# Performance work log

Hardware: AMD Instinct MI355X
Metric: run time of the kernel (lower is better)

Reference implementation:

```python
import jax, jax.numpy as jnp
import numpy as np

EPS = 1e-12  # guard sqrt at zero distance


def setup_inputs() -> dict:
    key = jax.random.key(0)
    k1, k2 = jax.random.split(key)
    B, C, N = 4, 3, 8192
    predict_pc = jax.random.normal(k1, (B, C, N), dtype=jnp.float32)
    gt_pc = jax.random.normal(k2, (B, C, N), dtype=jnp.float32)
    return {"predict_pc": predict_pc, "gt_pc": gt_pc}


def reference(predict_pc, gt_pc):
    # predict_pc: [B, 3, Np], gt_pc: [B, 3, Ng]
    B = gt_pc.shape[0]
    Np = predict_pc.shape[2]
    Ng = gt_pc.shape[2]
    denom = B * (Ng + Np)

    # Pairwise Euclidean distances d[b, n, m] = ||predict[b,:,n] - gt[b,:,m]||
    # via the |p|^2 + |g|^2 - 2 p.g expansion (avoids [B,3,Np,Ng] intermediate).
    p2 = jnp.sum(predict_pc * predict_pc, axis=1)            # [B, Np]
    g2 = jnp.sum(gt_pc * gt_pc, axis=1)                      # [B, Ng]
    dot = jnp.einsum('bcn,bcm->bnm', predict_pc, gt_pc)      # [B, Np, Ng]
    d2 = p2[:, :, None] + g2[:, None, :] - 2.0 * dot         # [B, Np, Ng]
    d = jnp.sqrt(jnp.maximum(d2, EPS))

    # z: for each gt point, distance to nearest predicted point -> min over Np
    z = jnp.min(d, axis=1)   # [B, Ng]
    # z_2: for each predicted point, distance to nearest gt point -> min over Ng
    z2 = jnp.min(d, axis=2)  # [B, Np]

    loss = z.sum() / denom + z2.sum() / denom
    return loss
```

## Files before the change

kernel.cpp:

```cpp
#include <hip/hip_runtime.h>
#include <math.h>


#define B_       4
#define N_       8192
#define THREADS  256
#define RX       8
#define XB       (THREADS * RX)
#define XBLKS    (N_ / XB)
#define NPB      (2 * B_)
#define RTHREADS 128

typedef float v2f __attribute__((ext_vector_type(2)));

__device__ __forceinline__ v2f pk_fma(v2f a, v2f b, v2f c) {
    v2f d;
    asm("v_pk_fma_f32 %0, %1, %2, %3" : "=v"(d) : "v"(a), "v"(b), "v"(c));
    return d;
}

__device__ __forceinline__ float min3f(float a, float b, float c) {
    float d;
    asm("v_min3_f32 %0, %1, %2, %3" : "=v"(d) : "v"(a), "v"(b), "v"(c));
    return d;
}


template<int YSPL>
__global__ __launch_bounds__(THREADS)
void chamfer_sweep_t(const float* __restrict__ P, const float* __restrict__ G,
                     float* __restrict__ partial)
{
    constexpr int YCHUNK = N_ / YSPL;
    constexpr int NJJ    = YCHUNK / 2;
    __shared__ float4 ytile[2 * NJJ];

    const int t      = threadIdx.x;
    const int xblk   = blockIdx.x;
    const int ysplit = blockIdx.y;
    const int bz     = blockIdx.z;
    const int pass   = bz >> 2;
    const int b      = bz & 3;

    const float* Xb = (pass ? G : P) + (size_t)b * 3 * N_;
    const float* Yb = (pass ? P : G) + (size_t)b * 3 * N_;

    const int ybase = ysplit * YCHUNK;
    if (t < NJJ) {
        const int n0 = ybase + 2 * t;
        float2 x01 = *(const float2*)&Yb[n0];
        float2 y01 = *(const float2*)&Yb[N_ + n0];
        float2 z01 = *(const float2*)&Yb[2 * N_ + n0];
        float w0 = fmaf(x01.x, x01.x, fmaf(y01.x, y01.x, z01.x * z01.x));
        float w1 = fmaf(x01.y, x01.y, fmaf(y01.y, y01.y, z01.y * z01.y));
        ytile[2 * t]     = make_float4(x01.x, x01.y, y01.x, y01.y);
        ytile[2 * t + 1] = make_float4(z01.x, z01.y, w0, w1);
    }

    const int xbase = xblk * XB;
    v2f m2x2[RX], m2y2[RX], m2z2[RX];
    float mn[RX];
#pragma unroll
    for (int r = 0; r < RX; ++r) {
        const int n = xbase + r * THREADS + t;
        float px = Xb[n];
        float py = Xb[N_ + n];
        float pz = Xb[2 * N_ + n];
        float ax = -2.0f * px, ay = -2.0f * py, az = -2.0f * pz;
        m2x2[r] = (v2f){ax, ax};
        m2y2[r] = (v2f){ay, ay};
        m2z2[r] = (v2f){az, az};
        mn[r]   = 3.4e38f;
    }
    __syncthreads();

#pragma unroll
    for (int jj = 0; jj < NJJ; ++jj) {
        float4 a4 = ytile[2 * jj];
        float4 b4 = ytile[2 * jj + 1];
        v2f gx2 = (v2f){a4.x, a4.y};
        v2f gy2 = (v2f){a4.z, a4.w};
        v2f gz2 = (v2f){b4.x, b4.y};
        v2f gw2 = (v2f){b4.z, b4.w};
#pragma unroll
        for (int r = 0; r < RX; ++r) {
            v2f s = pk_fma(m2z2[r], gz2, gw2);
            s = pk_fma(m2y2[r], gy2, s);
            s = pk_fma(m2x2[r], gx2, s);
            mn[r] = min3f(mn[r], s.x, s.y);
        }
    }

    float* pout = partial + ((size_t)bz * YSPL + ysplit) * N_ + xbase;
#pragma unroll
    for (int r = 0; r < RX; ++r) {
        float ax = m2x2[r].x, ay = m2y2[r].x, az = m2z2[r].x;
        float p2 = 0.25f * fmaf(ax, ax, fmaf(ay, ay, az * az));
        pout[r * THREADS + t] = fmaxf(mn[r] + p2, 1e-12f);
    }
}

template<int YSPL>
__global__ __launch_bounds__(RTHREADS)
void chamfer_reduce1_t(const float* __restrict__ partial,
                       float* __restrict__ gsum2)
{
    __shared__ float red[RTHREADS];
    const int g  = blockIdx.x * RTHREADS + threadIdx.x;
    const int pb = g >> 11;
    const int xq = g & 2047;
    const float4* p = (const float4*)(partial + (size_t)pb * YSPL * N_) + xq;
    float4 m = p[0];
#pragma unroll
    for (int ys = 1; ys < YSPL; ++ys) {
        float4 v = p[(size_t)ys * (N_ / 4)];
        m.x = fminf(m.x, v.x); m.y = fminf(m.y, v.y);
        m.z = fminf(m.z, v.z); m.w = fminf(m.w, v.w);
    }
    red[threadIdx.x] = sqrtf(m.x) + sqrtf(m.y) + sqrtf(m.z) + sqrtf(m.w);
    __syncthreads();
    for (int off = RTHREADS / 2; off > 0; off >>= 1) {
        if (threadIdx.x < off) red[threadIdx.x] += red[threadIdx.x + off];
        __syncthreads();
    }
    if (threadIdx.x == 0) gsum2[blockIdx.x] = red[0];
}

__global__ __launch_bounds__(RTHREADS)
void chamfer_final_kernel(const float* __restrict__ gsum2, float* __restrict__ out)
{
    __shared__ float red[RTHREADS];
    red[threadIdx.x] = gsum2[threadIdx.x];
    __syncthreads();
    for (int off = RTHREADS / 2; off > 0; off >>= 1) {
        if (threadIdx.x < off) red[threadIdx.x] += red[threadIdx.x + off];
        __syncthreads();
    }
    if (threadIdx.x == 0) out[0] = red[0] * (1.0f / 65536.0f);
}

#define LRX      8
#define LXB      (THREADS * LRX)
#define LXBLKS   (N_ / LXB)
#define LYSPL    32
#define LYCHUNK  (N_ / LYSPL)
#define LNGROUPS (2 * B_ * LXBLKS)
#define POISON   0xAAAAAAAAu

__global__ __launch_bounds__(THREADS)
void chamfer_fused_kernel(const float* __restrict__ P, const float* __restrict__ G,
                          unsigned* __restrict__ mins, unsigned* __restrict__ gcnt,
                          unsigned* __restrict__ fcnt, float* __restrict__ gsum,
                          float* __restrict__ out)
{
    __shared__ float4 ytile[2 * (LYCHUNK / 2)];
    __shared__ float red[THREADS];
    __shared__ unsigned s_ticket;

    const int t      = threadIdx.x;
    const int xblk   = blockIdx.x;
    const int ysplit = blockIdx.y;
    const int bz     = blockIdx.z;
    const int pass   = bz >> 2;
    const int b      = bz & 3;
    const int gid    = bz * LXBLKS + xblk;

    const float* Xb = (pass ? G : P) + (size_t)b * 3 * N_;
    const float* Yb = (pass ? P : G) + (size_t)b * 3 * N_;

    const int ybase = ysplit * LYCHUNK;
    if (t < LYCHUNK / 2) {
        const int n0 = ybase + 2 * t;
        float2 x01 = *(const float2*)&Yb[n0];
        float2 y01 = *(const float2*)&Yb[N_ + n0];
        float2 z01 = *(const float2*)&Yb[2 * N_ + n0];
        float w0 = fmaf(x01.x, x01.x, fmaf(y01.x, y01.x, z01.x * z01.x));
        float w1 = fmaf(x01.y, x01.y, fmaf(y01.y, y01.y, z01.y * z01.y));
        ytile[2 * t]     = make_float4(x01.x, x01.y, y01.x, y01.y);
        ytile[2 * t + 1] = make_float4(z01.x, z01.y, w0, w1);
    }

    const int xbase = xblk * LXB;
    v2f m2x2[LRX], m2y2[LRX], m2z2[LRX];
    float p2[LRX], mn[LRX];
#pragma unroll
    for (int r = 0; r < LRX; ++r) {
        const int n = xbase + r * THREADS + t;
        float px = Xb[n];
        float py = Xb[N_ + n];
        float pz = Xb[2 * N_ + n];
        p2[r]   = fmaf(px, px, fmaf(py, py, pz * pz));
        float ax = -2.0f * px, ay = -2.0f * py, az = -2.0f * pz;
        m2x2[r] = (v2f){ax, ax};
        m2y2[r] = (v2f){ay, ay};
        m2z2[r] = (v2f){az, az};
        mn[r]   = 3.4e38f;
    }
    __syncthreads();

#pragma unroll 2
    for (int jj = 0; jj < LYCHUNK / 2; ++jj) {
        float4 a4 = ytile[2 * jj];
        float4 b4 = ytile[2 * jj + 1];
        v2f gx2 = (v2f){a4.x, a4.y};
        v2f gy2 = (v2f){a4.z, a4.w};
        v2f gz2 = (v2f){b4.x, b4.y};
        v2f gw2 = (v2f){b4.z, b4.w};
#pragma unroll
        for (int r = 0; r < LRX; ++r) {
            v2f s = pk_fma(m2z2[r], gz2, gw2);
            s = pk_fma(m2y2[r], gy2, s);
            s = pk_fma(m2x2[r], gx2, s);
            mn[r] = fminf(fminf(mn[r], s.x), s.y);
        }
    }

    unsigned* mybase = mins + (size_t)(pass * B_ + b) * N_ + xbase;
#pragma unroll
    for (int r = 0; r < LRX; ++r) {
        float v = fmaxf(mn[r] + p2[r], 1e-12f);
        atomicMin(&mybase[r * THREADS + t], __float_as_uint(v));
    }

    __syncthreads();
    if (t == 0) {
        __threadfence();
        s_ticket = atomicAdd(&gcnt[gid], 1u);
    }
    __syncthreads();
    if (s_ticket != POISON + (unsigned)(LYSPL - 1)) return;

    __threadfence();
    const uint4* vmin = (const uint4*)(mins + (size_t)(pass * B_ + b) * N_ + xbase);
    uint4 q0 = vmin[t];
    uint4 q1 = vmin[THREADS + t];
    float a = sqrtf(__uint_as_float(q0.x)) + sqrtf(__uint_as_float(q0.y))
            + sqrtf(__uint_as_float(q0.z)) + sqrtf(__uint_as_float(q0.w))
            + sqrtf(__uint_as_float(q1.x)) + sqrtf(__uint_as_float(q1.y))
            + sqrtf(__uint_as_float(q1.z)) + sqrtf(__uint_as_float(q1.w));
    red[t] = a;
    __syncthreads();
    for (int off = 128; off > 0; off >>= 1) {
        if (t < off) red[t] += red[t + off];
        __syncthreads();
    }
    if (t == 0) {
        gsum[gid] = red[0];
        __threadfence();
        s_ticket = atomicAdd(fcnt, 1u);
    }
    __syncthreads();
    if (s_ticket != POISON + (unsigned)(LNGROUPS - 1)) return;

    __threadfence();
    red[t] = (t < LNGROUPS) ? gsum[t] : 0.0f;
    __syncthreads();
    for (int off = 128; off > 0; off >>= 1) {
        if (t < off) red[t] += red[t + off];
        __syncthreads();
    }
    if (t == 0) out[0] = red[0] * (1.0f / 65536.0f);
}

extern "C" void kernel_launch(void* const* d_in, const int* in_sizes, int n_in,
                              void* d_out, int out_size, void* d_ws, size_t ws_size,
                              hipStream_t stream)
{
    const float* P = (const float*)d_in[0];
    const float* G = (const float*)d_in[1];
    float* out = (float*)d_out;

    const size_t need64 = ((size_t)NPB * 64 * N_ + 256) * 4;
    const size_t need32 = ((size_t)NPB * 32 * N_ + 256) * 4;

    if (ws_size >= need64) {
        float* partial = (float*)d_ws;
        float* gsum2   = partial + (size_t)NPB * 64 * N_;
        chamfer_sweep_t<64><<<dim3(XBLKS, 64, NPB), THREADS, 0, stream>>>(P, G, partial);
        chamfer_reduce1_t<64><<<dim3(128), RTHREADS, 0, stream>>>(partial, gsum2);
        chamfer_final_kernel<<<dim3(1), RTHREADS, 0, stream>>>(gsum2, out);
    } else if (ws_size >= need32) {
        float* partial = (float*)d_ws;
        float* gsum2   = partial + (size_t)NPB * 32 * N_;
        chamfer_sweep_t<32><<<dim3(XBLKS, 32, NPB), THREADS, 0, stream>>>(P, G, partial);
        chamfer_reduce1_t<32><<<dim3(128), RTHREADS, 0, stream>>>(partial, gsum2);
        chamfer_final_kernel<<<dim3(1), RTHREADS, 0, stream>>>(gsum2, out);
    } else {
        unsigned* w    = (unsigned*)d_ws;
        unsigned* mins = w;
        unsigned* gcnt = w + 65536;
        unsigned* fcnt = w + 65600;
        float*    gsum = (float*)(w + 65664);
        dim3 grid(LXBLKS, LYSPL, NPB);
        chamfer_fused_kernel<<<grid, THREADS, 0, stream>>>(P, G, mins, gcnt, fcnt, gsum, out);
    }
}
```

Baseline: 106.2 us.

## Fuse both chamfer directions into one sweep exploiting distance symmetry

Replaces the two separate sweeps (P->G and G->P) with one sweep that computes each pairwise distance once. It keeps the row minima in registers and reduces column minima across threads through a double-buffered shared-memory tile plus wave shuffles, writing per-block column partials. A separate reduce kernel then folds the column partials. This aims to halve the FMA work, at the cost of extra adds, mins, shared-memory traffic and per-chunk barriers inside the inner loop.

```diff
diff --git a/kernel.cpp b/kernel.cpp
--- a/kernel.cpp
+++ b/kernel.cpp
@@ -8,8 +8,17 @@
 #define RX       8
 #define XB       (THREADS * RX)
 #define XBLKS    (N_ / XB)
-#define NPB      (2 * B_)
+#define YS       64
+#define YCHUNK   (N_ / YS)
+#define NJJ      (YCHUNK / 2)
 #define RTHREADS 128
+
+#define OFF_PX   0
+#define SZ_PX    ((size_t)B_ * YS * N_)
+#define OFF_PY   SZ_PX
+#define SZ_PY    ((size_t)B_ * XBLKS * N_)
+#define OFF_GS   (OFF_PY + SZ_PY)
+#define WORDS_NEED (OFF_GS + 128)
 
 typedef float v2f __attribute__((ext_vector_type(2)));
 
@@ -26,26 +35,22 @@
 }
 
 
-template<int YSPL>
 __global__ __launch_bounds__(THREADS)
-void chamfer_sweep_t(const float* __restrict__ P, const float* __restrict__ G,
-                     float* __restrict__ partial)
-{
-    constexpr int YCHUNK = N_ / YSPL;
-    constexpr int NJJ    = YCHUNK / 2;
+void chamfer_fused_sweep(const float* __restrict__ P, const float* __restrict__ G,
+                         float* __restrict__ partialX, float* __restrict__ partialY)
+{
     __shared__ float4 ytile[2 * NJJ];
-
-    const int t      = threadIdx.x;
-    const int xblk   = blockIdx.x;
-    const int ysplit = blockIdx.y;
-    const int bz     = blockIdx.z;
-    const int pass   = bz >> 2;
-    const int b      = bz & 3;
-
-    const float* Xb = (pass ? G : P) + (size_t)b * 3 * N_;
-    const float* Yb = (pass ? P : G) + (size_t)b * 3 * N_;
-
-    const int ybase = ysplit * YCHUNK;
+    __shared__ v2f    ybuf[2][8][THREADS];
+
+    const int t    = threadIdx.x;
+    const int xblk = blockIdx.x;
+    const int ys   = blockIdx.y;
+    const int b    = blockIdx.z;
+
+    const float* Xb = P + (size_t)b * 3 * N_;
+    const float* Yb = G + (size_t)b * 3 * N_;
+
+    const int ybase = ys * YCHUNK;
     if (t < NJJ) {
         const int n0 = ybase + 2 * t;
         float2 x01 = *(const float2*)&Yb[n0];
@@ -59,13 +64,14 @@
 
     const int xbase = xblk * XB;
     v2f m2x2[RX], m2y2[RX], m2z2[RX];
-    float mn[RX];
+    float p2[RX], mn[RX];
 #pragma unroll
     for (int r = 0; r < RX; ++r) {
         const int n = xbase + r * THREADS + t;
         float px = Xb[n];
         float py = Xb[N_ + n];
         float pz = Xb[2 * N_ + n];
+        p2[r]   = fmaf(px, px, fmaf(py, py, pz * pz));
         float ax = -2.0f * px, ay = -2.0f * py, az = -2.0f * pz;
         m2x2[r] = (v2f){ax, ax};
         m2y2[r] = (v2f){ay, ay};
@@ -74,45 +80,92 @@
     }
     __syncthreads();
 
-#pragma unroll
-    for (int jj = 0; jj < NJJ; ++jj) {
-        float4 a4 = ytile[2 * jj];
-        float4 b4 = ytile[2 * jj + 1];
-        v2f gx2 = (v2f){a4.x, a4.y};
-        v2f gy2 = (v2f){a4.z, a4.w};
-        v2f gz2 = (v2f){b4.x, b4.y};
-        v2f gw2 = (v2f){b4.z, b4.w};
-#pragma unroll
-        for (int r = 0; r < RX; ++r) {
-            v2f s = pk_fma(m2z2[r], gz2, gw2);
-            s = pk_fma(m2y2[r], gy2, s);
-            s = pk_fma(m2x2[r], gx2, s);
-            mn[r] = min3f(mn[r], s.x, s.y);
-        }
-    }
-
-    float* pout = partial + ((size_t)bz * YSPL + ysplit) * N_ + xbase;
-#pragma unroll
-    for (int r = 0; r < RX; ++r) {
-        float ax = m2x2[r].x, ay = m2y2[r].x, az = m2z2[r].x;
-        float p2 = 0.25f * fmaf(ax, ax, fmaf(ay, ay, az * az));
-        pout[r * THREADS + t] = fmaxf(mn[r] + p2, 1e-12f);
-    }
-}
-
-template<int YSPL>
+    for (int p = 0; p < 8; ++p) {
+#pragma unroll
+        for (int jo = 0; jo < 8; ++jo) {
+            const int jj = p * 8 + jo;
+            float4 a4 = ytile[2 * jj];
+            float4 b4 = ytile[2 * jj + 1];
+            v2f gx2 = (v2f){a4.x, a4.y};
+            v2f gy2 = (v2f){a4.z, a4.w};
+            v2f gz2 = (v2f){b4.x, b4.y};
+            v2f gw2 = (v2f){b4.z, b4.w};
+            float fm0, fm1, pfx, pfy;
+#pragma unroll
+            for (int r = 0; r < RX; ++r) {
+                v2f s = pk_fma(m2z2[r], gz2, gw2);
+                s = pk_fma(m2y2[r], gy2, s);
+                s = pk_fma(m2x2[r], gx2, s);
+                mn[r] = min3f(mn[r], s.x, s.y);
+                float fx = s.x + p2[r];
+                float fy = s.y + p2[r];
+                if (r == 0)      { pfx = fx; pfy = fy; }
+                else if (r == 1) { fm0 = fminf(pfx, fx); fm1 = fminf(pfy, fy); }
+                else if (r & 1)  { fm0 = min3f(fm0, pfx, fx); fm1 = min3f(fm1, pfy, fy); }
+                else             { pfx = fx; pfy = fy; }
+            }
+            ybuf[p & 1][jo][t] = (v2f){fm0, fm1};
+        }
+        if (p > 0) {
+            const int q = p - 1;
+            const int g = t >> 5, lane = t & 31;
+            v2f m = ybuf[q & 1][g][lane];
+#pragma unroll
+            for (int k = 1; k < 8; ++k) {
+                v2f v = ybuf[q & 1][g][lane + 32 * k];
+                m.x = fminf(m.x, v.x); m.y = fminf(m.y, v.y);
+            }
+#pragma unroll
+            for (int mask = 16; mask >= 1; mask >>= 1) {
+                m.x = fminf(m.x, __shfl_xor(m.x, mask));
+                m.y = fminf(m.y, __shfl_xor(m.y, mask));
+            }
+            if (lane == 0) {
+                const int y0 = ybase + 2 * (q * 8 + g);
+                *(float2*)&partialY[((size_t)b * XBLKS + xblk) * N_ + y0] =
+                    make_float2(m.x, m.y);
+            }
+        }
+        __syncthreads();
+    }
+    {
+        const int q = 7;
+        const int g = t >> 5, lane = t & 31;
+        v2f m = ybuf[q & 1][g][lane];
+#pragma unroll
+        for (int k = 1; k < 8; ++k) {
+            v2f v = ybuf[q & 1][g][lane + 32 * k];
+            m.x = fminf(m.x, v.x); m.y = fminf(m.y, v.y);
+        }
+#pragma unroll
+        for (int mask = 16; mask >= 1; mask >>= 1) {
+            m.x = fminf(m.x, __shfl_xor(m.x, mask));
+            m.y = fminf(m.y, __shfl_xor(m.y, mask));
+        }
+        if (lane == 0) {
+            const int y0 = ybase + 2 * (q * 8 + g);
+            *(float2*)&partialY[((size_t)b * XBLKS + xblk) * N_ + y0] =
+                make_float2(m.x, m.y);
+        }
+    }
+
+    float* pout = partialX + ((size_t)b * YS + ys) * N_ + xbase;
+#pragma unroll
+    for (int r = 0; r < RX; ++r)
+        pout[r * THREADS + t] = fmaxf(mn[r] + p2[r], 1e-12f);
+}
+
 __global__ __launch_bounds__(RTHREADS)
-void chamfer_reduce1_t(const float* __restrict__ partial,
-                       float* __restrict__ gsum2)
+void chamfer_reduceX(const float* __restrict__ partialX, float* __restrict__ gsum2)
 {
     __shared__ float red[RTHREADS];
-    const int g  = blockIdx.x * RTHREADS + threadIdx.x;
-    const int pb = g >> 11;
-    const int xq = g & 2047;
-    const float4* p = (const float4*)(partial + (size_t)pb * YSPL * N_) + xq;
+    const int g = blockIdx.x * RTHREADS + threadIdx.x;
+    const int b = g >> 11;
+    const int q = g & 2047;
+    const float4* p = (const float4*)(partialX + (size_t)b * YS * N_) + q;
     float4 m = p[0];
 #pragma unroll
-    for (int ys = 1; ys < YSPL; ++ys) {
+    for (int ys = 1; ys < YS; ++ys) {
         float4 v = p[(size_t)ys * (N_ / 4)];
         m.x = fminf(m.x, v.x); m.y = fminf(m.y, v.y);
         m.z = fminf(m.z, v.z); m.w = fminf(m.w, v.w);
@@ -124,6 +177,32 @@
         __syncthreads();
     }
     if (threadIdx.x == 0) gsum2[blockIdx.x] = red[0];
+}
+
+__global__ __launch_bounds__(RTHREADS)
+void chamfer_reduceY(const float* __restrict__ partialY, float* __restrict__ gsum2)
+{
+    __shared__ float red[RTHREADS];
+    const int g = blockIdx.x * RTHREADS + threadIdx.x;
+    const int b = g >> 11;
+    const int q = g & 2047;
+    const float4* p = (const float4*)(partialY + (size_t)b * XBLKS * N_) + q;
+    float4 m = p[0];
+#pragma unroll
+    for (int xt = 1; xt < XBLKS; ++xt) {
+        float4 v = p[(size_t)xt * (N_ / 4)];
+        m.x = fminf(m.x, v.x); m.y = fminf(m.y, v.y);
+        m.z = fminf(m.z, v.z); m.w = fminf(m.w, v.w);
+    }
+    m.x = fmaxf(m.x, 1e-12f); m.y = fmaxf(m.y, 1e-12f);
+    m.z = fmaxf(m.z, 1e-12f); m.w = fmaxf(m.w, 1e-12f);
+    red[threadIdx.x] = sqrtf(m.x) + sqrtf(m.y) + sqrtf(m.z) + sqrtf(m.w);
+    __syncthreads();
+    for (int off = RTHREADS / 2; off > 0; off >>= 1) {
+        if (threadIdx.x < off) red[threadIdx.x] += red[threadIdx.x + off];
+        __syncthreads();
+    }
+    if (threadIdx.x == 0) gsum2[64 + blockIdx.x] = red[0];
 }
 
 __global__ __launch_bounds__(RTHREADS)
@@ -270,20 +349,14 @@
     const float* G = (const float*)d_in[1];
     float* out = (float*)d_out;
 
-    const size_t need64 = ((size_t)NPB * 64 * N_ + 256) * 4;
-    const size_t need32 = ((size_t)NPB * 32 * N_ + 256) * 4;
-
-    if (ws_size >= need64) {
-        float* partial = (float*)d_ws;
-        float* gsum2   = partial + (size_t)NPB * 64 * N_;
-        chamfer_sweep_t<64><<<dim3(XBLKS, 64, NPB), THREADS, 0, stream>>>(P, G, partial);
-        chamfer_reduce1_t<64><<<dim3(128), RTHREADS, 0, stream>>>(partial, gsum2);
-        chamfer_final_kernel<<<dim3(1), RTHREADS, 0, stream>>>(gsum2, out);
-    } else if (ws_size >= need32) {
-        float* partial = (float*)d_ws;
-        float* gsum2   = partial + (size_t)NPB * 32 * N_;
-        chamfer_sweep_t<32><<<dim3(XBLKS, 32, NPB), THREADS, 0, stream>>>(P, G, partial);
-        chamfer_reduce1_t<32><<<dim3(128), RTHREADS, 0, stream>>>(partial, gsum2);
+    if (ws_size >= (size_t)WORDS_NEED * 4) {
+        float* wsf      = (float*)d_ws;
+        float* partialX = wsf + OFF_PX;
+        float* partialY = wsf + OFF_PY;
+        float* gsum2    = wsf + OFF_GS;
+        chamfer_fused_sweep<<<dim3(XBLKS, YS, B_), THREADS, 0, stream>>>(P, G, partialX, partialY);
+        chamfer_reduceX<<<dim3(64), RTHREADS, 0, stream>>>(partialX, gsum2);
+        chamfer_reduceY<<<dim3(64), RTHREADS, 0, stream>>>(partialY, gsum2);
         chamfer_final_kernel<<<dim3(1), RTHREADS, 0, stream>>>(gsum2, out);
     } else {
         unsigned* w    = (unsigned*)d_ws;
@@ -291,7 +364,7 @@
         unsigned* gcnt = w + 65536;
         unsigned* fcnt = w + 65600;
         float*    gsum = (float*)(w + 65664);
-        dim3 grid(LXBLKS, LYSPL, NPB);
+        dim3 grid(LXBLKS, LYSPL, 2 * B_);
         chamfer_fused_kernel<<<grid, THREADS, 0, stream>>>(P, G, mins, gcnt, fcnt, gsum, out);
     }
 }
```

After: 99.37 us. -6.4%, faster.
